# Kernel optimization log

Hardware: AMD Instinct MI355X
Metric: run time of the kernel (lower is better)

Reference implementation:

```python
import jax, jax.numpy as jnp
import numpy as np


def gcn_conv(x, W, b, src, dst, num_nodes):
    # h = X W  (tiny GEMM)
    h = x @ W
    # symmetric degree normalization with self-loops: D^-1/2 (A+I) D^-1/2
    deg = jax.ops.segment_sum(jnp.ones_like(dst, dtype=h.dtype), dst, num_segments=num_nodes)
    dinv = jnp.where(deg > 0, jax.lax.rsqrt(jnp.maximum(deg, 1e-12)), 0.0)
    norm = dinv[src] * dinv[dst]                      # [E]
    msg = h[src] * norm[:, None]                      # gather + scale, [E, F]
    out = jax.ops.segment_sum(msg, dst, num_segments=num_nodes)  # scatter-add, [N, F]
    return out + b


def reference(x, edge_index, W1, b1, W2, b2):
    num_nodes = x.shape[0]
    # add self-loops once (PyG GCNConv adds them inside each conv; identical edges both layers)
    loop = jnp.arange(num_nodes, dtype=edge_index.dtype)
    src = jnp.concatenate([edge_index[0], loop])
    dst = jnp.concatenate([edge_index[1], loop])
    h = gcn_conv(x, W1, b1, src, dst, num_nodes)
    h = jax.nn.relu(h)
    out = gcn_conv(h, W2, b2, src, dst, num_nodes)
    return out


def setup_inputs() -> dict:
    key = jax.random.key(0)
    k1, k2, k3, k4 = jax.random.split(key, 4)
    N, E, C_in, C_hid, C_out = 100000, 3200000, 128, 16, 128
    x = jax.random.normal(k1, (N, C_in), dtype=jnp.float32)
    edge_index = jax.random.randint(k2, (2, E), 0, N, dtype=jnp.int64)
    W1 = jax.random.normal(k3, (C_in, C_hid), dtype=jnp.float32) * (1.0 / np.sqrt(C_in))
    b1 = jnp.zeros((C_hid,), dtype=jnp.float32)
    W2 = jax.random.normal(k4, (C_hid, C_out), dtype=jnp.float32) * (1.0 / np.sqrt(C_hid))
    b2 = jnp.zeros((C_out,), dtype=jnp.float32)
    return {"x": x, "edge_index": edge_index, "W1": W1, "b1": b1, "W2": W2, "b2": b2}
```

## Files before the change

### kernel.cpp

```cpp
#include <hip/hip_runtime.h>
#include <hip/hip_fp16.h>

typedef _Float16 half8 __attribute__((ext_vector_type(8)));
typedef _Float16 half4 __attribute__((ext_vector_type(4)));
typedef float f32x4 __attribute__((ext_vector_type(4)));
typedef unsigned uint4v __attribute__((ext_vector_type(4)));

#define RANGE    512
#define RSH      9
#define CAP      17408
#define T_TILE   4096

__global__ void init_gcursor(int* __restrict__ gcursor, int NB) {
    int t = blockIdx.x * blockDim.x + threadIdx.x;
    if (t < NB) gcursor[t] = t * CAP;
}


__device__ __forceinline__ void unp8(uint4v v, float* f) {
#pragma unroll
    for (int k = 0; k < 4; ++k) {
        unsigned w = v[k];
        __half2 h2 = *reinterpret_cast<__half2*>(&w);
        float2 t = __half22float2(h2);
        f[2 * k] = t.x; f[2 * k + 1] = t.y;
    }
}

__device__ __forceinline__ void acc8(float* a, uint4v v) {
#pragma unroll
    for (int k = 0; k < 4; ++k) {
        unsigned w = v[k];
        __half2 h2 = *reinterpret_cast<__half2*>(&w);
        float2 t = __half22float2(h2);
        a[2 * k]     += t.x;
        a[2 * k + 1] += t.y;
    }
}

__device__ __forceinline__ uint4v pk8(const float* o) {
    uint4v r;
#pragma unroll
    for (int k = 0; k < 4; ++k) {
        __half2 h2 = __floats2half2_rn(o[2 * k], o[2 * k + 1]);
        r[k] = *reinterpret_cast<unsigned*>(&h2);
    }
    return r;
}


__global__ __launch_bounds__(256) void binpass_gemm1(const int* __restrict__ src,
                                                     const int* __restrict__ dst, int E,
                                                     int* __restrict__ gcursor,
                                                     unsigned* __restrict__ pairbuf,
                                                     int binBlocks,
                                                     const float* __restrict__ x,
                                                     const float* __restrict__ W1,
                                                     __half* __restrict__ g1, int N) {
    if (blockIdx.x >= binBlocks) {
        int wave = threadIdx.x >> 6;
        int lane = threadIdx.x & 63;
        int R0 = (blockIdx.x - binBlocks) * 64 + wave * 16;
        if (R0 >= N) return;
        int m = lane & 15;
        int kb = (lane >> 4) * 8;
        int row = R0 + m;
        int rowc = min(row, N - 1);

        half8 bfrag[4];
#pragma unroll
        for (int kk = 0; kk < 4; ++kk) {
#pragma unroll
            for (int j = 0; j < 8; ++j)
                bfrag[kk][j] = (_Float16)W1[(kk * 32 + kb + j) * 16 + m];
        }
        const float* xr = x + (size_t)rowc * 128;
        float4 u[8];
#pragma unroll
        for (int kk = 0; kk < 4; ++kk) {
            u[2 * kk]     = *reinterpret_cast<const float4*>(xr + kk * 32 + kb);
            u[2 * kk + 1] = *reinterpret_cast<const float4*>(xr + kk * 32 + kb + 4);
        }
        f32x4 acc = {0.f, 0.f, 0.f, 0.f};
#pragma unroll
        for (int kk = 0; kk < 4; ++kk) {
            half8 a;
            a[0] = (_Float16)u[2 * kk].x;     a[1] = (_Float16)u[2 * kk].y;
            a[2] = (_Float16)u[2 * kk].z;     a[3] = (_Float16)u[2 * kk].w;
            a[4] = (_Float16)u[2 * kk + 1].x; a[5] = (_Float16)u[2 * kk + 1].y;
            a[6] = (_Float16)u[2 * kk + 1].z; a[7] = (_Float16)u[2 * kk + 1].w;
            acc = __builtin_amdgcn_mfma_f32_16x16x32_f16(a, bfrag[kk], acc, 0, 0, 0);
        }
#pragma unroll
        for (int i = 0; i < 4; ++i) {
            int r = R0 + (lane >> 4) * 4 + i;
            if (r < N) g1[(size_t)r * 16 + m] = __float2half(acc[i]);
        }
        return;
    }
    __shared__ unsigned sbuf[T_TILE];
    __shared__ unsigned char sbk[T_TILE];
    __shared__ int lcount[256], loff[256], lplace[256], gbase[256];
    int t = threadIdx.x;
    int base = blockIdx.x * T_TILE;
    int ecount = min(T_TILE, E - base);

    lcount[t] = 0;
    __syncthreads();

    unsigned pk[16];
    int bn[16];
#pragma unroll
    for (int k4 = 0; k4 < 4; ++k4) {
        int i = base + (t + k4 * 256) * 4;
        if (i + 3 < E) {
            int4 sv = *reinterpret_cast<const int4*>(src + i);
            int4 dv = *reinterpret_cast<const int4*>(dst + i);
            int ss[4] = {sv.x, sv.y, sv.z, sv.w};
            int dd[4] = {dv.x, dv.y, dv.z, dv.w};
#pragma unroll
            for (int m = 0; m < 4; ++m) {
                int k = k4 * 4 + m;
                bn[k] = dd[m] >> RSH;
                pk[k] = ((unsigned)ss[m] << RSH) | (unsigned)(dd[m] & (RANGE - 1));
                atomicAdd(&lcount[bn[k]], 1);
            }
        } else {
#pragma unroll
            for (int m = 0; m < 4; ++m) {
                int k = k4 * 4 + m;
                int ii = i + m;
                if (ii < E) {
                    int s = src[ii], d = dst[ii];
                    bn[k] = d >> RSH;
                    pk[k] = ((unsigned)s << RSH) | (unsigned)(d & (RANGE - 1));
                    atomicAdd(&lcount[bn[k]], 1);
                } else bn[k] = -1;
            }
        }
    }
    __syncthreads();
    loff[t] = lcount[t];
    __syncthreads();
    for (int off = 1; off < 256; off <<= 1) {
        int u = (t >= off) ? loff[t - off] : 0;
        __syncthreads();
        loff[t] += u;
        __syncthreads();
    }
    int ex = loff[t] - lcount[t];
    __syncthreads();
    loff[t] = ex;
    lplace[t] = ex;
    if (lcount[t] > 0) gbase[t] = atomicAdd(&gcursor[t], lcount[t]);
    __syncthreads();
#pragma unroll
    for (int k = 0; k < 16; ++k) {
        if (bn[k] >= 0) {
            int pos = atomicAdd(&lplace[bn[k]], 1);
            sbuf[pos] = pk[k];
            sbk[pos] = (unsigned char)bn[k];
        }
    }
    __syncthreads();
    for (int i = t; i < ecount; i += 256) {
        int b = sbk[i];
        pairbuf[gbase[b] + (i - loff[b])] = sbuf[i];
    }
}


__global__ __launch_bounds__(512) void bucket_build(const unsigned* __restrict__ pairbuf,
                                                    const int* __restrict__ gcursor,
                                                    int NB, int N, int E,
                                                    int* __restrict__ rowptr,
                                                    float* __restrict__ dinv,
                                                    int* __restrict__ eidx,
                                                    __half* __restrict__ g1,
                                                    __half* __restrict__ g2) {
    __shared__ unsigned spair[CAP];
    __shared__ int lcnt[RANGE];
    __shared__ int lsc[RANGE];
    __shared__ int sscan[256];
    int b = blockIdx.x, t = threadIdx.x;

    if (t < 256) sscan[t] = (t < NB) ? (gcursor[t] - t * CAP) : 0;
    if (t < RANGE) lcnt[t] = 0;
    __syncthreads();
    for (int off = 1; off < 256; off <<= 1) {
        int u = (t >= off && t < 256) ? sscan[t - off] : 0;
        __syncthreads();
        if (t < 256) sscan[t] += u;
        __syncthreads();
    }
    int gb = (b == 0) ? 0 : sscan[b - 1];
    int cnt = gcursor[b] - b * CAP;
    const unsigned* pb = pairbuf + (size_t)b * CAP;

    for (int i = t; i < cnt; i += 512) {
        unsigned p = pb[i];
        spair[i] = p;
        atomicAdd(&lcnt[p & (RANGE - 1)], 1);
    }
    __syncthreads();
    lsc[t] = lcnt[t];
    __syncthreads();
    for (int off = 1; off < 512; off <<= 1) {
        int u = (t >= off) ? lsc[t - off] : 0;
        __syncthreads();
        lsc[t] += u;
        __syncthreads();
    }
    int ex = lsc[t] - lcnt[t];
    int node = b * RANGE + t;
    if (node < N) {
        rowptr[node] = gb + ex;
        float di = rsqrtf((float)lcnt[t] + 1.0f);
        dinv[node] = di;
        __half* gr = g1 + (size_t)node * 16;
        uint4v v0 = *reinterpret_cast<const uint4v*>(gr);
        uint4v v1 = *reinterpret_cast<const uint4v*>(gr + 8);
        float f[8];
        unp8(v0, f);
#pragma unroll
        for (int k = 0; k < 8; ++k) f[k] *= di;
        *reinterpret_cast<uint4v*>(gr) = pk8(f);
        unp8(v1, f);
#pragma unroll
        for (int k = 0; k < 8; ++k) f[k] *= di;
        *reinterpret_cast<uint4v*>(gr + 8) = pk8(f);
    } else if (node == N) {
        uint4v z = {0u, 0u, 0u, 0u};
        *reinterpret_cast<uint4v*>(g1 + (size_t)N * 16)     = z;
        *reinterpret_cast<uint4v*>(g1 + (size_t)N * 16 + 8) = z;
        *reinterpret_cast<uint4v*>(g2 + (size_t)N * 16)     = z;
        *reinterpret_cast<uint4v*>(g2 + (size_t)N * 16 + 8) = z;
    }
    if (b == 0 && t == 0) rowptr[N] = E;
    __syncthreads();
    lsc[t] = gb + ex;
    __syncthreads();
    for (int i = t; i < cnt; i += 512) {
        unsigned p = spair[i];
        int pos = atomicAdd(&lsc[p & (RANGE - 1)], 1);
        eidx[pos] = (int)(p >> RSH);
    }
}


__global__ __launch_bounds__(256) void gather1_kernel(const int* __restrict__ rowptr,
                                                      const int* __restrict__ eidx,
                                                      const __half* __restrict__ g1,
                                                      const float* __restrict__ dinv,
                                                      const float* __restrict__ b1,
                                                      __half* __restrict__ g2, int N) {
    int gid = blockIdx.x * blockDim.x + threadIdx.x;
    int d = gid >> 3;
    if (d >= N) return;
    int sub = threadIdx.x & 7;
    int h = sub & 1, es = sub >> 1;
    int f0 = h * 8;
    int lo = rowptr[d], hi = rowptr[d + 1];
    float di = dinv[d];
    uint4v svh = *reinterpret_cast<const uint4v*>(g1 + (size_t)d * 16 + f0);

    float a[8] = {0, 0, 0, 0, 0, 0, 0, 0};
    for (int j = lo + es; j < hi; j += 32) {
        int idx[8];
#pragma unroll
        for (int k = 0; k < 8; ++k) {
            int jj = j + 4 * k;
            idx[k] = (jj < hi) ? eidx[jj] : N;
        }
        uint4v v[8];
#pragma unroll
        for (int k = 0; k < 8; ++k)
            v[k] = *reinterpret_cast<const uint4v*>(g1 + (size_t)idx[k] * 16 + f0);
#pragma unroll
        for (int k = 0; k < 8; ++k) acc8(a, v[k]);
    }
#pragma unroll
    for (int k = 0; k < 8; ++k) {
        a[k] += __shfl_xor(a[k], 2);
        a[k] += __shfl_xor(a[k], 4);
    }
    if (es == 0) {
        float sf[8];
        unp8(svh, sf);
        f32x4 bb0 = *reinterpret_cast<const f32x4*>(b1 + f0);
        f32x4 bb1 = *reinterpret_cast<const f32x4*>(b1 + f0 + 4);
        float o[8];
#pragma unroll
        for (int k = 0; k < 4; ++k) {
            o[k]     = fmaxf(di * (a[k] + sf[k]) + bb0[k], 0.0f) * di;
            o[k + 4] = fmaxf(di * (a[k + 4] + sf[k + 4]) + bb1[k], 0.0f) * di;
        }
        *reinterpret_cast<uint4v*>(g2 + (size_t)d * 16 + f0) = pk8(o);
    }
}


__global__ __launch_bounds__(256) void gather2_gemm2(const int* __restrict__ rowptr,
                                                     const int* __restrict__ eidx,
                                                     const __half* __restrict__ g2,
                                                     const float* __restrict__ dinv,
                                                     const float* __restrict__ W2,
                                                     const float* __restrict__ b2,
                                                     float* __restrict__ out, int N) {
    int gid = blockIdx.x * blockDim.x + threadIdx.x;
    int wid = gid >> 6;
    int lane = threadIdx.x & 63;
    int base = wid * 16;
    if (base >= N) return;
    int nl = lane & 15;
    int q = lane >> 4;
    int es = q & 1;
    int h = lane >> 5;
    int f0 = h * 8;
    int d = base + nl;
    int dc = min(d, N - 1);
    int lo = rowptr[dc], hi = rowptr[dc + 1];
    float di = dinv[dc];
    uint4v sv = *reinterpret_cast<const uint4v*>(g2 + (size_t)dc * 16 + f0);

    float a[8] = {0, 0, 0, 0, 0, 0, 0, 0};
    for (int j = lo + es; j < hi; j += 16) {
        int idx[8];
#pragma unroll
        for (int k = 0; k < 8; ++k) {
            int jj = j + 2 * k;
            idx[k] = (jj < hi) ? eidx[jj] : N;
        }
        uint4v v[8];
#pragma unroll
        for (int k = 0; k < 8; ++k)
            v[k] = *reinterpret_cast<const uint4v*>(g2 + (size_t)idx[k] * 16 + f0);
#pragma unroll
        for (int k = 0; k < 8; ++k) acc8(a, v[k]);
    }
#pragma unroll
    for (int k = 0; k < 8; ++k) a[k] += __shfl_xor(a[k], 16);

    float sf[8];
    unp8(sv, sf);
    float af[8];
#pragma unroll
    for (int k = 0; k < 8; ++k) af[k] = di * (a[k] + sf[k]);

    int hi4 = es * 4;
    half4 afrag;
#pragma unroll
    for (int jj = 0; jj < 4; ++jj) afrag[jj] = (_Float16)af[hi4 + jj];

    f32x4 dacc[8];
#pragma unroll
    for (int ct = 0; ct < 8; ++ct) {
        half4 bfrag;
#pragma unroll
        for (int jj = 0; jj < 4; ++jj)
            bfrag[jj] = (_Float16)W2[(q * 4 + jj) * 128 + ct * 16 + nl];
        f32x4 z = {0.f, 0.f, 0.f, 0.f};
        dacc[ct] = __builtin_amdgcn_mfma_f32_16x16x16f16(afrag, bfrag, z, 0, 0, 0);
    }

    float bias[8];
#pragma unroll
    for (int ct = 0; ct < 8; ++ct) bias[ct] = b2[ct * 16 + nl];

    int rbase = base + q * 4;
#pragma unroll
    for (int i = 0; i < 4; ++i) {
        int r = rbase + i;
        if (r < N) {
            float* orow = out + (size_t)r * 128 + nl;
#pragma unroll
            for (int ct = 0; ct < 8; ++ct) orow[ct * 16] = dacc[ct][i] + bias[ct];
        }
    }
}


extern "C" void kernel_launch(void* const* d_in, const int* in_sizes, int n_in,
                              void* d_out, int out_size, void* d_ws, size_t ws_size,
                              hipStream_t stream) {
    const float* x  = (const float*)d_in[0];
    const int*   ei = (const int*)d_in[1];
    const float* W1 = (const float*)d_in[2];
    const float* b1 = (const float*)d_in[3];
    const float* W2 = (const float*)d_in[4];
    const float* b2 = (const float*)d_in[5];
    float* out = (float*)d_out;

    const int N = in_sizes[0] / 128;
    const int E = in_sizes[1] / 2;
    const int* src = ei;
    const int* dst = ei + E;
    const int NB = (N + RANGE - 1) / RANGE;

    unsigned* pairbuf = (unsigned*)d_ws;
    int* gcursor = (int*)(pairbuf + (size_t)NB * CAP);
    int* rowptr  = gcursor + NB;
    int* eidx    = rowptr + (N + 1);
    float* dinv  = (float*)(eidx + E);
    __half* g1 = (__half*)(dinv + N);
    __half* g2 = g1 + 16 * (N + 1);

    const int B = 256;
    const int binBlocks  = (E + T_TILE - 1) / T_TILE;
    const int gemmBlocks = (N + 63) / 64;
    init_gcursor<<<1, B, 0, stream>>>(gcursor, NB);
    binpass_gemm1<<<binBlocks + gemmBlocks, B, 0, stream>>>(src, dst, E, gcursor, pairbuf,
                                                            binBlocks, x, W1, g1, N);
    bucket_build<<<NB, 512, 0, stream>>>(pairbuf, gcursor, NB, N, E, rowptr, dinv, eidx, g1, g2);
    gather1_kernel<<<(N * 8 + B - 1) / B, B, 0, stream>>>(rowptr, eidx, g1, dinv, b1, g2, N);
    gather2_gemm2<<<(N * 4 + B - 1) / B, B, 0, stream>>>(rowptr, eidx, g2, dinv, W2, b2, out, N);
}
```

Baseline: 132.2 us.

## Split fused layer-2 gather+GEMM into separate gather and MFMA GEMM kernels

```diff
diff --git a/kernel.cpp b/kernel.cpp
--- a/kernel.cpp
+++ b/kernel.cpp
@@ -300,57 +300,66 @@
 }
 
 
-__global__ __launch_bounds__(256) void gather2_gemm2(const int* __restrict__ rowptr,
-                                                     const int* __restrict__ eidx,
-                                                     const __half* __restrict__ g2,
-                                                     const float* __restrict__ dinv,
-                                                     const float* __restrict__ W2,
-                                                     const float* __restrict__ b2,
-                                                     float* __restrict__ out, int N) {
+__global__ __launch_bounds__(256) void gather2_kernel(const int* __restrict__ rowptr,
+                                                      const int* __restrict__ eidx,
+                                                      const __half* __restrict__ g2,
+                                                      const float* __restrict__ dinv,
+                                                      __half* __restrict__ g3, int N) {
     int gid = blockIdx.x * blockDim.x + threadIdx.x;
-    int wid = gid >> 6;
+    int d = gid >> 3;
+    if (d >= N) return;
+    int sub = threadIdx.x & 7;
+    int h = sub & 1, es = sub >> 1;
+    int f0 = h * 8;
+    int lo = rowptr[d], hi = rowptr[d + 1];
+    float di = dinv[d];
+    uint4v svh = *reinterpret_cast<const uint4v*>(g2 + (size_t)d * 16 + f0);
+
+    float a[8] = {0, 0, 0, 0, 0, 0, 0, 0};
+    for (int j = lo + es; j < hi; j += 32) {
+        int idx[8];
+#pragma unroll
+        for (int k = 0; k < 8; ++k) {
+            int jj = j + 4 * k;
+            idx[k] = (jj < hi) ? eidx[jj] : N;
+        }
+        uint4v v[8];
+#pragma unroll
+        for (int k = 0; k < 8; ++k)
+            v[k] = *reinterpret_cast<const uint4v*>(g2 + (size_t)idx[k] * 16 + f0);
+#pragma unroll
+        for (int k = 0; k < 8; ++k) acc8(a, v[k]);
+    }
+#pragma unroll
+    for (int k = 0; k < 8; ++k) {
+        a[k] += __shfl_xor(a[k], 2);
+        a[k] += __shfl_xor(a[k], 4);
+    }
+    if (es == 0) {
+        float sf[8];
+        unp8(svh, sf);
+        float o[8];
+#pragma unroll
+        for (int k = 0; k < 8; ++k) o[k] = di * (a[k] + sf[k]);
+        *reinterpret_cast<uint4v*>(g3 + (size_t)d * 16 + f0) = pk8(o);
+    }
+}
+
+
+__global__ __launch_bounds__(256) void gemm2_mfma(const __half* __restrict__ g3,
+                                                  const float* __restrict__ W2,
+                                                  const float* __restrict__ b2,
+                                                  float* __restrict__ out, int N) {
+    int wave = threadIdx.x >> 6;
     int lane = threadIdx.x & 63;
-    int base = wid * 16;
-    if (base >= N) return;
+    int R0 = blockIdx.x * 64 + wave * 16;
+    if (R0 >= N) return;
     int nl = lane & 15;
     int q = lane >> 4;
-    int es = q & 1;
-    int h = lane >> 5;
-    int f0 = h * 8;
-    int d = base + nl;
-    int dc = min(d, N - 1);
-    int lo = rowptr[dc], hi = rowptr[dc + 1];
-    float di = dinv[dc];
-    uint4v sv = *reinterpret_cast<const uint4v*>(g2 + (size_t)dc * 16 + f0);
-
-    float a[8] = {0, 0, 0, 0, 0, 0, 0, 0};
-    for (int j = lo + es; j < hi; j += 16) {
-        int idx[8];
-#pragma unroll
-        for (int k = 0; k < 8; ++k) {
-            int jj = j + 2 * k;
-            idx[k] = (jj < hi) ? eidx[jj] : N;
-        }
-        uint4v v[8];
-#pragma unroll
-        for (int k = 0; k < 8; ++k)
-            v[k] = *reinterpret_cast<const uint4v*>(g2 + (size_t)idx[k] * 16 + f0);
-#pragma unroll
-        for (int k = 0; k < 8; ++k) acc8(a, v[k]);
-    }
-#pragma unroll
-    for (int k = 0; k < 8; ++k) a[k] += __shfl_xor(a[k], 16);
-
-    float sf[8];
-    unp8(sv, sf);
-    float af[8];
-#pragma unroll
-    for (int k = 0; k < 8; ++k) af[k] = di * (a[k] + sf[k]);
-
-    int hi4 = es * 4;
-    half4 afrag;
-#pragma unroll
-    for (int jj = 0; jj < 4; ++jj) afrag[jj] = (_Float16)af[hi4 + jj];
+    int row = R0 + nl;
+    int rowc = min(row, N - 1);
+
+    half4 afrag = *reinterpret_cast<const half4*>(g3 + (size_t)rowc * 16 + q * 4);
 
     f32x4 dacc[8];
 #pragma unroll
@@ -367,7 +376,7 @@
 #pragma unroll
     for (int ct = 0; ct < 8; ++ct) bias[ct] = b2[ct * 16 + nl];
 
-    int rbase = base + q * 4;
+    int rbase = R0 + q * 4;
 #pragma unroll
     for (int i = 0; i < 4; ++i) {
         int r = rbase + i;
@@ -404,6 +413,7 @@
     float* dinv  = (float*)(eidx + E);
     __half* g1 = (__half*)(dinv + N);
     __half* g2 = g1 + 16 * (N + 1);
+    __half* g3 = g2 + 16 * (N + 1);
 
     const int B = 256;
     const int binBlocks  = (E + T_TILE - 1) / T_TILE;
@@ -413,5 +423,6 @@
                                                             binBlocks, x, W1, g1, N);
     bucket_build<<<NB, 512, 0, stream>>>(pairbuf, gcursor, NB, N, E, rowptr, dinv, eidx, g1, g2);
     gather1_kernel<<<(N * 8 + B - 1) / B, B, 0, stream>>>(rowptr, eidx, g1, dinv, b1, g2, N);
-    gather2_gemm2<<<(N * 4 + B - 1) / B, B, 0, stream>>>(rowptr, eidx, g2, dinv, W2, b2, out, N);
-}
+    gather2_kernel<<<(N * 8 + B - 1) / B, B, 0, stream>>>(rowptr, eidx, g2, dinv, g3, N);
+    gemm2_mfma<<<gemmBlocks, B, 0, stream>>>(g3, W2, b2, out, N);
+}
```

After: 127.8 us. -3.3%, faster.
